# Performance work log

Hardware: AMD Instinct MI355X
Metric: run time of the kernel (lower is better)

Reference implementation:

```python
import jax, jax.numpy as jnp
import numpy as np

B, S, D = 8, 1024, 768
H = 12
DH = D // H  # 64


def setup_inputs() -> dict:
    key = jax.random.key(0)
    ks = jax.random.split(key, 9)
    s = 0.02
    return {
        "x": jax.random.normal(ks[0], (B, S, D), dtype=jnp.float32),
        # per-head QKV projections stacked over heads: [H, D, DH]
        "Wq": jax.random.normal(ks[1], (H, D, DH), dtype=jnp.float32) * s,
        "bq": jax.random.normal(ks[2], (H, DH), dtype=jnp.float32) * s,
        "Wk": jax.random.normal(ks[3], (H, D, DH), dtype=jnp.float32) * s,
        "bk": jax.random.normal(ks[4], (H, DH), dtype=jnp.float32) * s,
        "Wv": jax.random.normal(ks[5], (H, D, DH), dtype=jnp.float32) * s,
        "bv": jax.random.normal(ks[6], (H, DH), dtype=jnp.float32) * s,
        # output projection: [D, D] (applied as x @ Wo + bo)
        "Wo": jax.random.normal(ks[7], (D, D), dtype=jnp.float32) * s,
        "bo": jax.random.normal(ks[8], (D,), dtype=jnp.float32) * s,
    }


def reference(x, Wq, bq, Wk, bk, Wv, bv, Wo, bo):
    # Per-head linear projections, vectorized over heads -> [B, H, S, DH]
    q = jnp.einsum("bsd,hde->bhse", x, Wq) + bq[None, :, None, :]
    k = jnp.einsum("bsd,hde->bhse", x, Wk) + bk[None, :, None, :]
    v = jnp.einsum("bsd,hde->bhse", x, Wv) + bv[None, :, None, :]
    scale = 1.0 / jnp.sqrt(jnp.asarray(DH, dtype=q.dtype))
    scores = jnp.einsum("bhse,bhte->bhst", q, k) * scale  # [B,H,S,S]
    probs = jax.nn.softmax(scores, axis=-1)  # dropout p=0 (eval)
    out = jnp.einsum("bhst,bhte->bhse", probs, v)  # [B,H,S,DH]
    # concat heads (head order matches ModuleList order) -> [B,S,D]
    out = out.transpose(0, 2, 1, 3).reshape(B, S, D)
    return out @ Wo + bo
```

## Files before the change

### kernel.cpp

```cpp
#include <hip/hip_runtime.h>
#include <math.h>

#define BB 8
#define SS 1024
#define DD 768
#define HH 12
#define DHH 64
#define BSS (BB*SS)
#define NQKV 2304

typedef _Float16 half8 __attribute__((ext_vector_type(8)));
typedef _Float16 half4 __attribute__((ext_vector_type(4)));
typedef float    f32x4 __attribute__((ext_vector_type(4)));

__device__ __forceinline__ void glds16(const _Float16* g, _Float16* l)
{
    __builtin_amdgcn_global_load_lds(
        (const __attribute__((address_space(1))) uint32_t*)(g),
        (__attribute__((address_space(3))) uint32_t*)(l),
        16, 0, 0);
}

__global__ __launch_bounds__(256)
void cast_x_f16(const float* __restrict__ x, _Float16* __restrict__ xh)
{
    int i = blockIdx.x * 256 + threadIdx.x;
    const float4* xp = (const float4*)x + (size_t)i * 2;
    float4 u = xp[0], v = xp[1];
    half8 h = { (_Float16)u.x, (_Float16)u.y, (_Float16)u.z, (_Float16)u.w,
                (_Float16)v.x, (_Float16)v.y, (_Float16)v.z, (_Float16)v.w };
    ((half8*)xh)[i] = h;
}

__device__ __forceinline__
void transpose_tile(const float* __restrict__ src, _Float16* __restrict__ dst,
                    int d0, int n_outer, int base_mul, int row_stride, int tid)
{
    __shared__ float T[64][65];
    const size_t base = (size_t)n_outer * base_mul;
    {
        int dl = tid >> 2, c0 = (tid & 3) * 16;
        const float* p = src + base + (size_t)(d0 + dl) * row_stride + c0;
#pragma unroll
        for (int m = 0; m < 4; ++m) {
            float4 f = *(const float4*)(p + m * 4);
            T[dl][c0 + m*4 + 0] = f.x;
            T[dl][c0 + m*4 + 1] = f.y;
            T[dl][c0 + m*4 + 2] = f.z;
            T[dl][c0 + m*4 + 3] = f.w;
        }
    }
    __syncthreads();
    {
        int e = tid >> 2, c = tid & 3;
        half8 lo, hi;
#pragma unroll
        for (int i = 0; i < 8; ++i) {
            lo[i] = (_Float16)T[c*16 + i][e];
            hi[i] = (_Float16)T[c*16 + 8 + i][e];
        }
        _Float16* q = dst + ((size_t)n_outer * 64 + e) * DD + d0 + c * 16;
        *(half8*)q = lo;
        *(half8*)(q + 8) = hi;
    }
}

__global__ __launch_bounds__(256)
void transpose_all(const float* __restrict__ Wq, const float* __restrict__ Wk,
                   const float* __restrict__ Wv, const float* __restrict__ Wo,
                   _Float16* __restrict__ Wt, _Float16* __restrict__ Wot)
{
    const int z = blockIdx.z;
    const float* src;
    _Float16* dst;
    int base_mul, row_stride;
    if (z < 3) {
        src = (z == 0) ? Wq : (z == 1) ? Wk : Wv;
        dst = Wt + (size_t)z * DD * DD;
        base_mul = DD * DHH; row_stride = DHH;
    } else {
        src = Wo; dst = Wot;
        base_mul = 64; row_stride = DD;
    }
    transpose_tile(src, dst, blockIdx.x * 64, blockIdx.y, base_mul, row_stride,
                   threadIdx.x);
}

__global__ __launch_bounds__(256)
void gemm_qkv_stacked(const _Float16* __restrict__ Xh, const _Float16* __restrict__ Wt,
                      const float* __restrict__ bq, const float* __restrict__ bk,
                      const float* __restrict__ bv,
                      _Float16* __restrict__ qo, _Float16* __restrict__ ko,
                      _Float16* __restrict__ vto)
{
    __shared__ _Float16 Ash[128][32];
    __shared__ _Float16 Bsh[128][32];

    const int b = blockIdx.x;
    const int c  = b & 7;
    const int g  = b >> 3;
    const int n_t = g % 18;
    const int m_t = (g / 18) * 8 + c;
    const int m0 = m_t * 128;
    const int n0 = n_t * 128;

    const int tid  = threadIdx.x;
    const int wave = tid >> 6;
    const int lane = tid & 63;
    const int l16  = tid & 15;
    const int quad = (tid >> 4) & 3;
    const int wy = wave >> 1;
    const int wx = wave & 1;

    const _Float16* ap = Xh + (size_t)(m0 + 32 * wave + (lane >> 2)) * DD + (lane & 3) * 8;
    const _Float16* bp = Wt + (size_t)(n0 + 32 * wave + (lane >> 2)) * DD + (lane & 3) * 8;
    _Float16* ldsA0 = &Ash[32 * wave][0];
    _Float16* ldsA1 = &Ash[32 * wave + 16][0];
    _Float16* ldsB0 = &Bsh[32 * wave][0];
    _Float16* ldsB1 = &Bsh[32 * wave + 16][0];

    f32x4 acc[4][4];
#pragma unroll
    for (int i = 0; i < 4; ++i)
#pragma unroll
        for (int j = 0; j < 4; ++j) acc[i][j] = (f32x4){0.f, 0.f, 0.f, 0.f};

    for (int k0 = 0; k0 < DD; k0 += 32) {
        __syncthreads();
        glds16(ap, ldsA0);
        glds16(ap + 16 * DD, ldsA1);
        glds16(bp, ldsB0);
        glds16(bp + 16 * DD, ldsB1);
        ap += 32; bp += 32;
        __syncthreads();

        half8 a[4], bf[4];
#pragma unroll
        for (int i = 0; i < 4; ++i)
            a[i] = *(const half8*)&Ash[wy * 64 + i * 16 + l16][quad * 8];
#pragma unroll
        for (int j = 0; j < 4; ++j)
            bf[j] = *(const half8*)&Bsh[wx * 64 + j * 16 + l16][quad * 8];
#pragma unroll
        for (int i = 0; i < 4; ++i)
#pragma unroll
            for (int j = 0; j < 4; ++j)
                acc[i][j] = __builtin_amdgcn_mfma_f32_16x16x32_f16(a[i], bf[j], acc[i][j], 0, 0, 0);
    }

    const int w = n0 / 768;
    const float* bp_ = (w == 0) ? bq : (w == 1) ? bk : bv;
    const int nb = n0 - w * 768 + wx * 64;
    const float qscale = (w == 0) ? 0.125f : 1.0f;

#pragma unroll
    for (int i = 0; i < 4; ++i) {
#pragma unroll
        for (int r = 0; r < 4; ++r) {
            int row = m0 + wy * 64 + i * 16 + quad * 4 + r;
            int b_ = row >> 10;
            int s  = row & (SS - 1);
#pragma unroll
            for (int j = 0; j < 4; ++j) {
                int nl = nb + j * 16 + l16;
                int h = nl >> 6, e = nl & 63;
                float val = (acc[i][j][r] + bp_[nl]) * qscale;
                if (w == 0)
                    qo[((size_t)(b_ * HH + h) * SS + s) * DHH + e] = (_Float16)val;
                else if (w == 1)
                    ko[((size_t)(b_ * HH + h) * SS + s) * DHH + e] = (_Float16)val;
                else
                    vto[((size_t)(b_ * HH + h) * DHH + e) * SS + s] = (_Float16)val;
            }
        }
    }
}

__global__ __launch_bounds__(256)
void gemm_out_f16(const _Float16* __restrict__ Ah, const _Float16* __restrict__ Bt,
                  const float* __restrict__ bias, float* __restrict__ out)
{
    __shared__ _Float16 Ash[128][32];
    __shared__ _Float16 Bsh[128][32];

    const int m0 = blockIdx.x * 128;
    const int n0 = blockIdx.y * 128;
    const int tid  = threadIdx.x;
    const int wave = tid >> 6;
    const int lane = tid & 63;
    const int l16  = tid & 15;
    const int quad = (tid >> 4) & 3;
    const int wy = wave >> 1;
    const int wx = wave & 1;

    const _Float16* ap = Ah + (size_t)(m0 + 32 * wave + (lane >> 2)) * DD + (lane & 3) * 8;
    const _Float16* bp = Bt + (size_t)(n0 + 32 * wave + (lane >> 2)) * DD + (lane & 3) * 8;
    _Float16* ldsA0 = &Ash[32 * wave][0];
    _Float16* ldsA1 = &Ash[32 * wave + 16][0];
    _Float16* ldsB0 = &Bsh[32 * wave][0];
    _Float16* ldsB1 = &Bsh[32 * wave + 16][0];

    f32x4 acc[4][4];
#pragma unroll
    for (int i = 0; i < 4; ++i)
#pragma unroll
        for (int j = 0; j < 4; ++j) acc[i][j] = (f32x4){0.f, 0.f, 0.f, 0.f};

    for (int k0 = 0; k0 < DD; k0 += 32) {
        __syncthreads();
        glds16(ap, ldsA0);
        glds16(ap + 16 * DD, ldsA1);
        glds16(bp, ldsB0);
        glds16(bp + 16 * DD, ldsB1);
        ap += 32; bp += 32;
        __syncthreads();

        half8 a[4], bf[4];
#pragma unroll
        for (int i = 0; i < 4; ++i)
            a[i] = *(const half8*)&Ash[wy * 64 + i * 16 + l16][quad * 8];
#pragma unroll
        for (int j = 0; j < 4; ++j)
            bf[j] = *(const half8*)&Bsh[wx * 64 + j * 16 + l16][quad * 8];
#pragma unroll
        for (int i = 0; i < 4; ++i)
#pragma unroll
            for (int j = 0; j < 4; ++j)
                acc[i][j] = __builtin_amdgcn_mfma_f32_16x16x32_f16(a[i], bf[j], acc[i][j], 0, 0, 0);
    }

#pragma unroll
    for (int i = 0; i < 4; ++i) {
#pragma unroll
        for (int r = 0; r < 4; ++r) {
            int row = m0 + wy * 64 + i * 16 + quad * 4 + r;
#pragma unroll
            for (int j = 0; j < 4; ++j) {
                int col = n0 + wx * 64 + j * 16 + l16;
                out[(size_t)row * DD + col] = acc[i][j][r] + bias[col];
            }
        }
    }
}

__global__ __launch_bounds__(256)
void attn_f16(const _Float16* __restrict__ qh, const _Float16* __restrict__ kh,
              const _Float16* __restrict__ vt, _Float16* __restrict__ ctxh)
{
    const int bh  = blockIdx.x;
    const int q0  = blockIdx.y * 64;
    const int tid = threadIdx.x;
    const int wave = tid >> 6;
    const int lane = tid & 63;
    const int l16  = tid & 15;
    const int quad = (tid >> 4) & 3;

    __shared__ _Float16 Qs[64][64];
    __shared__ _Float16 Ks[64][64];
    __shared__ _Float16 Vt[64][64];
    __shared__ _Float16 Pt[4][16][72];

    const _Float16* qb  = qh + ((size_t)bh * SS + q0) * DHH;
    const _Float16* kb  = kh + (size_t)bh * SS * DHH;
    const _Float16* vtb = vt + (size_t)bh * DHH * SS;

    const int srow = 16 * wave + (lane >> 3);
    const int scol = (lane & 7) * 8;
    const _Float16* qp = qb + (size_t)srow * DHH + scol;
    const _Float16* kp = kb + (size_t)srow * DHH + scol;
    const _Float16* vp = vtb + (size_t)srow * SS + scol;

    glds16(qp, &Qs[16 * wave][0]);
    glds16(qp + 8 * DHH, &Qs[16 * wave + 8][0]);
    __syncthreads();

    const half8 qlo = *(const half8*)&Qs[wave * 16 + l16][quad * 8];
    const half8 qhi = *(const half8*)&Qs[wave * 16 + l16][32 + quad * 8];

    f32x4 o[4];
    float lacc = 0.f;
#pragma unroll
    for (int j = 0; j < 4; ++j) o[j] = (f32x4){0.f, 0.f, 0.f, 0.f};

    for (int kt = 0; kt < SS; kt += 64) {
        __syncthreads();
        glds16(kp, &Ks[16 * wave][0]);
        glds16(kp + 8 * DHH, &Ks[16 * wave + 8][0]);
        glds16(vp, &Vt[16 * wave][0]);
        glds16(vp + 8 * SS, &Vt[16 * wave + 8][0]);
        kp += 64 * DHH;
        vp += 64;
        __syncthreads();

#pragma unroll
        for (int f = 0; f < 4; ++f) {
            half8 klo = *(const half8*)&Ks[f * 16 + l16][quad * 8];
            half8 khi = *(const half8*)&Ks[f * 16 + l16][32 + quad * 8];
            f32x4 z = (f32x4){0.f, 0.f, 0.f, 0.f};
            z = __builtin_amdgcn_mfma_f32_16x16x32_f16(klo, qlo, z, 0, 0, 0);
            z = __builtin_amdgcn_mfma_f32_16x16x32_f16(khi, qhi, z, 0, 0, 0);
            half4 pk;
#pragma unroll
            for (int r = 0; r < 4; ++r) {
                float p = __expf(z[r]);
                lacc += p;
                pk[r] = (_Float16)p;
            }
            *(half4*)&Pt[wave][l16][f * 16 + quad * 4] = pk;
        }

        half8 pl = *(const half8*)&Pt[wave][l16][quad * 8];
        half8 ph = *(const half8*)&Pt[wave][l16][32 + quad * 8];

#pragma unroll
        for (int j = 0; j < 4; ++j) {
            half8 vlo = *(const half8*)&Vt[j * 16 + l16][quad * 8];
            half8 vhi = *(const half8*)&Vt[j * 16 + l16][32 + quad * 8];
            o[j] = __builtin_amdgcn_mfma_f32_16x16x32_f16(pl, vlo, o[j], 0, 0, 0);
            o[j] = __builtin_amdgcn_mfma_f32_16x16x32_f16(ph, vhi, o[j], 0, 0, 0);
        }
    }

    float lr = lacc;
    lr += __shfl_xor(lr, 16);
    lr += __shfl_xor(lr, 32);

    const int b_ = bh / HH;
    const int h_ = bh % HH;
#pragma unroll
    for (int r = 0; r < 4; ++r) {
        float invl = 1.f / __shfl(lr, quad * 4 + r, 16);
        int s_ = q0 + wave * 16 + quad * 4 + r;
        _Float16* orow = ctxh + ((size_t)(b_ * SS + s_)) * DD + h_ * DHH;
#pragma unroll
        for (int j = 0; j < 4; ++j)
            orow[j * 16 + l16] = (_Float16)(o[j][r] * invl);
    }
}

extern "C" void kernel_launch(void* const* d_in, const int* in_sizes, int n_in,
                              void* d_out, int out_size, void* d_ws, size_t ws_size,
                              hipStream_t stream)
{
    const float* x  = (const float*)d_in[0];
    const float* Wq = (const float*)d_in[1];
    const float* bq = (const float*)d_in[2];
    const float* Wk = (const float*)d_in[3];
    const float* bk = (const float*)d_in[4];
    const float* Wv = (const float*)d_in[5];
    const float* bv = (const float*)d_in[6];
    const float* Wo = (const float*)d_in[7];
    const float* bo = (const float*)d_in[8];
    float* out = (float*)d_out;

    const size_t xe = (size_t)BSS * DD;
    const size_t we = (size_t)DD * DD;
    _Float16* Xh   = (_Float16*)d_ws;
    _Float16* Wt   = Xh  + xe;
    _Float16* Wot  = Wt  + (size_t)3 * we;
    _Float16* qhb  = Wot + we;
    _Float16* khb  = qhb + xe;
    _Float16* vtb  = khb + xe;
    _Float16* ctxh = vtb + xe;

    cast_x_f16<<<xe / 8 / 256, 256, 0, stream>>>(x, Xh);

    dim3 tg(DD / 64, DD / 64, 4);
    transpose_all<<<tg, 256, 0, stream>>>(Wq, Wk, Wv, Wo, Wt, Wot);

    gemm_qkv_stacked<<<(BSS / 128) * (NQKV / 128), 256, 0, stream>>>(
        Xh, Wt, bq, bk, bv, qhb, khb, vtb);

    dim3 ag(BB * HH, SS / 64);
    attn_f16<<<ag, 256, 0, stream>>>(qhb, khb, vtb, ctxh);

    dim3 gg(BSS / 128, DD / 128);
    gemm_out_f16<<<gg, 256, 0, stream>>>(ctxh, Wot, bo, out);
}
```

Before: 240.1 us.

## Load GEMM and attention operands directly from global memory into registers

Drops the LDS staging and the per-iteration block barriers in both GEMMs and in the attention kernel. Each wave now reads its MFMA fragments straight from global memory, with register double-buffering to prefetch the next K slice. The output GEMM tile shrinks to 64 rows and launch bounds request 3 blocks per CU for occupancy. The cost is lost data sharing across waves: each A/B and K/V element is fetched from global or L2 several times, and the 16-byte per-lane row-strided loads may coalesce poorly.

```diff
diff --git a/kernel.cpp b/kernel.cpp
--- a/kernel.cpp
+++ b/kernel.cpp
@@ -12,14 +12,6 @@
 typedef _Float16 half8 __attribute__((ext_vector_type(8)));
 typedef _Float16 half4 __attribute__((ext_vector_type(4)));
 typedef float    f32x4 __attribute__((ext_vector_type(4)));
-
-__device__ __forceinline__ void glds16(const _Float16* g, _Float16* l)
-{
-    __builtin_amdgcn_global_load_lds(
-        (const __attribute__((address_space(1))) uint32_t*)(g),
-        (__attribute__((address_space(3))) uint32_t*)(l),
-        16, 0, 0);
-}
 
 __global__ __launch_bounds__(256)
 void cast_x_f16(const float* __restrict__ x, _Float16* __restrict__ xh)
@@ -86,16 +78,13 @@
                    threadIdx.x);
 }
 
-__global__ __launch_bounds__(256)
-void gemm_qkv_stacked(const _Float16* __restrict__ Xh, const _Float16* __restrict__ Wt,
-                      const float* __restrict__ bq, const float* __restrict__ bk,
-                      const float* __restrict__ bv,
-                      _Float16* __restrict__ qo, _Float16* __restrict__ ko,
-                      _Float16* __restrict__ vto)
-{
-    __shared__ _Float16 Ash[128][32];
-    __shared__ _Float16 Bsh[128][32];
-
+__global__ __launch_bounds__(256, 3)
+void gemm_qkv_direct(const _Float16* __restrict__ Xh, const _Float16* __restrict__ Wt,
+                     const float* __restrict__ bq, const float* __restrict__ bk,
+                     const float* __restrict__ bv,
+                     _Float16* __restrict__ qo, _Float16* __restrict__ ko,
+                     _Float16* __restrict__ vto)
+{
     const int b = blockIdx.x;
     const int c  = b & 7;
     const int g  = b >> 3;
@@ -106,18 +95,13 @@
 
     const int tid  = threadIdx.x;
     const int wave = tid >> 6;
-    const int lane = tid & 63;
     const int l16  = tid & 15;
     const int quad = (tid >> 4) & 3;
     const int wy = wave >> 1;
     const int wx = wave & 1;
 
-    const _Float16* ap = Xh + (size_t)(m0 + 32 * wave + (lane >> 2)) * DD + (lane & 3) * 8;
-    const _Float16* bp = Wt + (size_t)(n0 + 32 * wave + (lane >> 2)) * DD + (lane & 3) * 8;
-    _Float16* ldsA0 = &Ash[32 * wave][0];
-    _Float16* ldsA1 = &Ash[32 * wave + 16][0];
-    _Float16* ldsB0 = &Bsh[32 * wave][0];
-    _Float16* ldsB1 = &Bsh[32 * wave + 16][0];
+    const _Float16* abase = Xh + (size_t)(m0 + wy * 64 + l16) * DD + quad * 8;
+    const _Float16* bbase = Wt + (size_t)(n0 + wx * 64 + l16) * DD + quad * 8;
 
     f32x4 acc[4][4];
 #pragma unroll
@@ -125,27 +109,31 @@
 #pragma unroll
         for (int j = 0; j < 4; ++j) acc[i][j] = (f32x4){0.f, 0.f, 0.f, 0.f};
 
-    for (int k0 = 0; k0 < DD; k0 += 32) {
-        __syncthreads();
-        glds16(ap, ldsA0);
-        glds16(ap + 16 * DD, ldsA1);
-        glds16(bp, ldsB0);
-        glds16(bp + 16 * DD, ldsB1);
-        ap += 32; bp += 32;
-        __syncthreads();
-
-        half8 a[4], bf[4];
-#pragma unroll
-        for (int i = 0; i < 4; ++i)
-            a[i] = *(const half8*)&Ash[wy * 64 + i * 16 + l16][quad * 8];
-#pragma unroll
-        for (int j = 0; j < 4; ++j)
-            bf[j] = *(const half8*)&Bsh[wx * 64 + j * 16 + l16][quad * 8];
+    half8 a[4], bf[4];
+#pragma unroll
+    for (int i = 0; i < 4; ++i) {
+        a[i]  = *(const half8*)(abase + (size_t)i * 16 * DD);
+        bf[i] = *(const half8*)(bbase + (size_t)i * 16 * DD);
+    }
+
+    for (int k0 = 32; k0 <= DD; k0 += 32) {
+        half8 an[4], bn[4];
+        if (k0 < DD) {
+#pragma unroll
+            for (int i = 0; i < 4; ++i) {
+                an[i] = *(const half8*)(abase + (size_t)i * 16 * DD + k0);
+                bn[i] = *(const half8*)(bbase + (size_t)i * 16 * DD + k0);
+            }
+        }
 #pragma unroll
         for (int i = 0; i < 4; ++i)
 #pragma unroll
             for (int j = 0; j < 4; ++j)
                 acc[i][j] = __builtin_amdgcn_mfma_f32_16x16x32_f16(a[i], bf[j], acc[i][j], 0, 0, 0);
+        if (k0 < DD) {
+#pragma unroll
+            for (int i = 0; i < 4; ++i) { a[i] = an[i]; bf[i] = bn[i]; }
+        }
     }
 
     const int w = n0 / 768;
@@ -176,64 +164,60 @@
     }
 }
 
-__global__ __launch_bounds__(256)
-void gemm_out_f16(const _Float16* __restrict__ Ah, const _Float16* __restrict__ Bt,
-                  const float* __restrict__ bias, float* __restrict__ out)
-{
-    __shared__ _Float16 Ash[128][32];
-    __shared__ _Float16 Bsh[128][32];
-
-    const int m0 = blockIdx.x * 128;
+__global__ __launch_bounds__(256, 3)
+void gemm_out_direct(const _Float16* __restrict__ Ah, const _Float16* __restrict__ Bt,
+                     const float* __restrict__ bias, float* __restrict__ out)
+{
+    const int m0 = blockIdx.x * 64;
     const int n0 = blockIdx.y * 128;
     const int tid  = threadIdx.x;
     const int wave = tid >> 6;
-    const int lane = tid & 63;
     const int l16  = tid & 15;
     const int quad = (tid >> 4) & 3;
     const int wy = wave >> 1;
     const int wx = wave & 1;
 
-    const _Float16* ap = Ah + (size_t)(m0 + 32 * wave + (lane >> 2)) * DD + (lane & 3) * 8;
-    const _Float16* bp = Bt + (size_t)(n0 + 32 * wave + (lane >> 2)) * DD + (lane & 3) * 8;
-    _Float16* ldsA0 = &Ash[32 * wave][0];
-    _Float16* ldsA1 = &Ash[32 * wave + 16][0];
-    _Float16* ldsB0 = &Bsh[32 * wave][0];
-    _Float16* ldsB1 = &Bsh[32 * wave + 16][0];
-
-    f32x4 acc[4][4];
-#pragma unroll
-    for (int i = 0; i < 4; ++i)
+    const _Float16* abase = Ah + (size_t)(m0 + wy * 32 + l16) * DD + quad * 8;
+    const _Float16* bbase = Bt + (size_t)(n0 + wx * 64 + l16) * DD + quad * 8;
+
+    f32x4 acc[2][4];
+#pragma unroll
+    for (int i = 0; i < 2; ++i)
 #pragma unroll
         for (int j = 0; j < 4; ++j) acc[i][j] = (f32x4){0.f, 0.f, 0.f, 0.f};
 
-    for (int k0 = 0; k0 < DD; k0 += 32) {
-        __syncthreads();
-        glds16(ap, ldsA0);
-        glds16(ap + 16 * DD, ldsA1);
-        glds16(bp, ldsB0);
-        glds16(bp + 16 * DD, ldsB1);
-        ap += 32; bp += 32;
-        __syncthreads();
-
-        half8 a[4], bf[4];
-#pragma unroll
-        for (int i = 0; i < 4; ++i)
-            a[i] = *(const half8*)&Ash[wy * 64 + i * 16 + l16][quad * 8];
-#pragma unroll
-        for (int j = 0; j < 4; ++j)
-            bf[j] = *(const half8*)&Bsh[wx * 64 + j * 16 + l16][quad * 8];
-#pragma unroll
-        for (int i = 0; i < 4; ++i)
+    half8 a[2], bf[4];
+#pragma unroll
+    for (int i = 0; i < 2; ++i) a[i] = *(const half8*)(abase + (size_t)i * 16 * DD);
+#pragma unroll
+    for (int j = 0; j < 4; ++j) bf[j] = *(const half8*)(bbase + (size_t)j * 16 * DD);
+
+    for (int k0 = 32; k0 <= DD; k0 += 32) {
+        half8 an[2], bn[4];
+        if (k0 < DD) {
+#pragma unroll
+            for (int i = 0; i < 2; ++i) an[i] = *(const half8*)(abase + (size_t)i * 16 * DD + k0);
+#pragma unroll
+            for (int j = 0; j < 4; ++j) bn[j] = *(const half8*)(bbase + (size_t)j * 16 * DD + k0);
+        }
+#pragma unroll
+        for (int i = 0; i < 2; ++i)
 #pragma unroll
             for (int j = 0; j < 4; ++j)
                 acc[i][j] = __builtin_amdgcn_mfma_f32_16x16x32_f16(a[i], bf[j], acc[i][j], 0, 0, 0);
-    }
-
-#pragma unroll
-    for (int i = 0; i < 4; ++i) {
+        if (k0 < DD) {
+#pragma unroll
+            for (int i = 0; i < 2; ++i) a[i] = an[i];
+#pragma unroll
+            for (int j = 0; j < 4; ++j) bf[j] = bn[j];
+        }
+    }
+
+#pragma unroll
+    for (int i = 0; i < 2; ++i) {
 #pragma unroll
         for (int r = 0; r < 4; ++r) {
-            int row = m0 + wy * 64 + i * 16 + quad * 4 + r;
+            int row = m0 + wy * 32 + i * 16 + quad * 4 + r;
 #pragma unroll
             for (int j = 0; j < 4; ++j) {
                 int col = n0 + wx * 64 + j * 16 + l16;
@@ -251,31 +235,17 @@
     const int q0  = blockIdx.y * 64;
     const int tid = threadIdx.x;
     const int wave = tid >> 6;
-    const int lane = tid & 63;
     const int l16  = tid & 15;
     const int quad = (tid >> 4) & 3;
 
-    __shared__ _Float16 Qs[64][64];
-    __shared__ _Float16 Ks[64][64];
-    __shared__ _Float16 Vt[64][64];
     __shared__ _Float16 Pt[4][16][72];
 
-    const _Float16* qb  = qh + ((size_t)bh * SS + q0) * DHH;
-    const _Float16* kb  = kh + (size_t)bh * SS * DHH;
-    const _Float16* vtb = vt + (size_t)bh * DHH * SS;
-
-    const int srow = 16 * wave + (lane >> 3);
-    const int scol = (lane & 7) * 8;
-    const _Float16* qp = qb + (size_t)srow * DHH + scol;
-    const _Float16* kp = kb + (size_t)srow * DHH + scol;
-    const _Float16* vp = vtb + (size_t)srow * SS + scol;
-
-    glds16(qp, &Qs[16 * wave][0]);
-    glds16(qp + 8 * DHH, &Qs[16 * wave + 8][0]);
-    __syncthreads();
-
-    const half8 qlo = *(const half8*)&Qs[wave * 16 + l16][quad * 8];
-    const half8 qhi = *(const half8*)&Qs[wave * 16 + l16][32 + quad * 8];
+    const _Float16* qrow = qh + ((size_t)bh * SS + q0 + wave * 16 + l16) * DHH;
+    const half8 qlo = *(const half8*)(qrow + quad * 8);
+    const half8 qhi = *(const half8*)(qrow + 32 + quad * 8);
+
+    const _Float16* kptr = kh + ((size_t)bh * SS + l16) * DHH + quad * 8;
+    const _Float16* vptr = vt + ((size_t)bh * DHH + l16) * SS + quad * 8;
 
     f32x4 o[4];
     float lacc = 0.f;
@@ -283,22 +253,26 @@
     for (int j = 0; j < 4; ++j) o[j] = (f32x4){0.f, 0.f, 0.f, 0.f};
 
     for (int kt = 0; kt < SS; kt += 64) {
-        __syncthreads();
-        glds16(kp, &Ks[16 * wave][0]);
-        glds16(kp + 8 * DHH, &Ks[16 * wave + 8][0]);
-        glds16(vp, &Vt[16 * wave][0]);
-        glds16(vp + 8 * SS, &Vt[16 * wave + 8][0]);
-        kp += 64 * DHH;
-        vp += 64;
-        __syncthreads();
-
+        half8 kl[4], khv[4];
 #pragma unroll
         for (int f = 0; f < 4; ++f) {
-            half8 klo = *(const half8*)&Ks[f * 16 + l16][quad * 8];
-            half8 khi = *(const half8*)&Ks[f * 16 + l16][32 + quad * 8];
+            const _Float16* kp = kptr + (size_t)(kt + f * 16) * DHH;
+            kl[f]  = *(const half8*)kp;
+            khv[f] = *(const half8*)(kp + 32);
+        }
+        half8 vl[4], vh[4];
+#pragma unroll
+        for (int j = 0; j < 4; ++j) {
+            const _Float16* vp = vptr + (size_t)j * 16 * SS + kt;
+            vl[j] = *(const half8*)vp;
+            vh[j] = *(const half8*)(vp + 32);
+        }
+
+#pragma unroll
+        for (int f = 0; f < 4; ++f) {
             f32x4 z = (f32x4){0.f, 0.f, 0.f, 0.f};
-            z = __builtin_amdgcn_mfma_f32_16x16x32_f16(klo, qlo, z, 0, 0, 0);
-            z = __builtin_amdgcn_mfma_f32_16x16x32_f16(khi, qhi, z, 0, 0, 0);
+            z = __builtin_amdgcn_mfma_f32_16x16x32_f16(kl[f], qlo, z, 0, 0, 0);
+            z = __builtin_amdgcn_mfma_f32_16x16x32_f16(khv[f], qhi, z, 0, 0, 0);
             half4 pk;
 #pragma unroll
             for (int r = 0; r < 4; ++r) {
@@ -314,10 +288,8 @@
 
 #pragma unroll
         for (int j = 0; j < 4; ++j) {
-            half8 vlo = *(const half8*)&Vt[j * 16 + l16][quad * 8];
-            half8 vhi = *(const half8*)&Vt[j * 16 + l16][32 + quad * 8];
-            o[j] = __builtin_amdgcn_mfma_f32_16x16x32_f16(pl, vlo, o[j], 0, 0, 0);
-            o[j] = __builtin_amdgcn_mfma_f32_16x16x32_f16(ph, vhi, o[j], 0, 0, 0);
+            o[j] = __builtin_amdgcn_mfma_f32_16x16x32_f16(pl, vl[j], o[j], 0, 0, 0);
+            o[j] = __builtin_amdgcn_mfma_f32_16x16x32_f16(ph, vh[j], o[j], 0, 0, 0);
         }
     }
 
@@ -368,12 +340,12 @@
     dim3 tg(DD / 64, DD / 64, 4);
     transpose_all<<<tg, 256, 0, stream>>>(Wq, Wk, Wv, Wo, Wt, Wot);
 
-    gemm_qkv_stacked<<<(BSS / 128) * (NQKV / 128), 256, 0, stream>>>(
+    gemm_qkv_direct<<<(BSS / 128) * (NQKV / 128), 256, 0, stream>>>(
         Xh, Wt, bq, bk, bv, qhb, khb, vtb);
 
     dim3 ag(BB * HH, SS / 64);
     attn_f16<<<ag, 256, 0, stream>>>(qhb, khb, vtb, ctxh);
 
-    dim3 gg(BSS / 128, DD / 128);
-    gemm_out_f16<<<gg, 256, 0, stream>>>(ctxh, Wot, bo, out);
-}
+    dim3 gg(BSS / 64, DD / 128);
+    gemm_out_direct<<<gg, 256, 0, stream>>>(ctxh, Wot, bo, out);
+}
```

Result: slower. 467.7 us (+94.8%).

## Double-buffer LDS tiles in GEMMs and attention, widen attention blocks

Applied to the files above, without the earlier changes.

The QKV GEMM, output GEMM and attention kernels now use two LDS buffers. Each loop iteration prefetches the next K tile with async global-to-LDS loads while MFMAs run on the current tile, so each iteration needs one barrier instead of two. The attention kernel grows to 512 threads and 128 queries per block, which lets more query rows share each staged K/V tile; Q fragments are now read straight from global memory. The output GEMM tile shrinks to 128x64 to launch more blocks. In exchange, LDS use per block roughly doubles, which can lower occupancy.

```diff
diff --git a/kernel.cpp b/kernel.cpp
--- a/kernel.cpp
+++ b/kernel.cpp
@@ -93,8 +93,8 @@
                       _Float16* __restrict__ qo, _Float16* __restrict__ ko,
                       _Float16* __restrict__ vto)
 {
-    __shared__ _Float16 Ash[128][32];
-    __shared__ _Float16 Bsh[128][32];
+    __shared__ _Float16 Ash[2][128][32];
+    __shared__ _Float16 Bsh[2][128][32];
 
     const int b = blockIdx.x;
     const int c  = b & 7;
@@ -114,10 +114,6 @@
 
     const _Float16* ap = Xh + (size_t)(m0 + 32 * wave + (lane >> 2)) * DD + (lane & 3) * 8;
     const _Float16* bp = Wt + (size_t)(n0 + 32 * wave + (lane >> 2)) * DD + (lane & 3) * 8;
-    _Float16* ldsA0 = &Ash[32 * wave][0];
-    _Float16* ldsA1 = &Ash[32 * wave + 16][0];
-    _Float16* ldsB0 = &Bsh[32 * wave][0];
-    _Float16* ldsB1 = &Bsh[32 * wave + 16][0];
 
     f32x4 acc[4][4];
 #pragma unroll
@@ -125,27 +121,34 @@
 #pragma unroll
         for (int j = 0; j < 4; ++j) acc[i][j] = (f32x4){0.f, 0.f, 0.f, 0.f};
 
+    glds16(ap, &Ash[0][32 * wave][0]);
+    glds16(ap + 16 * DD, &Ash[0][32 * wave + 16][0]);
+    glds16(bp, &Bsh[0][32 * wave][0]);
+    glds16(bp + 16 * DD, &Bsh[0][32 * wave + 16][0]);
+
+    int cur = 0;
     for (int k0 = 0; k0 < DD; k0 += 32) {
         __syncthreads();
-        glds16(ap, ldsA0);
-        glds16(ap + 16 * DD, ldsA1);
-        glds16(bp, ldsB0);
-        glds16(bp + 16 * DD, ldsB1);
-        ap += 32; bp += 32;
-        __syncthreads();
+        if (k0 + 32 < DD) {
+            glds16(ap + k0 + 32, &Ash[cur ^ 1][32 * wave][0]);
+            glds16(ap + k0 + 32 + 16 * DD, &Ash[cur ^ 1][32 * wave + 16][0]);
+            glds16(bp + k0 + 32, &Bsh[cur ^ 1][32 * wave][0]);
+            glds16(bp + k0 + 32 + 16 * DD, &Bsh[cur ^ 1][32 * wave + 16][0]);
+        }
 
         half8 a[4], bf[4];
 #pragma unroll
         for (int i = 0; i < 4; ++i)
-            a[i] = *(const half8*)&Ash[wy * 64 + i * 16 + l16][quad * 8];
+            a[i] = *(const half8*)&Ash[cur][wy * 64 + i * 16 + l16][quad * 8];
 #pragma unroll
         for (int j = 0; j < 4; ++j)
-            bf[j] = *(const half8*)&Bsh[wx * 64 + j * 16 + l16][quad * 8];
+            bf[j] = *(const half8*)&Bsh[cur][wx * 64 + j * 16 + l16][quad * 8];
 #pragma unroll
         for (int i = 0; i < 4; ++i)
 #pragma unroll
             for (int j = 0; j < 4; ++j)
                 acc[i][j] = __builtin_amdgcn_mfma_f32_16x16x32_f16(a[i], bf[j], acc[i][j], 0, 0, 0);
+        cur ^= 1;
     }
 
     const int w = n0 / 768;
@@ -180,11 +183,11 @@
 void gemm_out_f16(const _Float16* __restrict__ Ah, const _Float16* __restrict__ Bt,
                   const float* __restrict__ bias, float* __restrict__ out)
 {
-    __shared__ _Float16 Ash[128][32];
-    __shared__ _Float16 Bsh[128][32];
+    __shared__ _Float16 Ash[2][128][32];
+    __shared__ _Float16 Bsh[2][64][32];
 
     const int m0 = blockIdx.x * 128;
-    const int n0 = blockIdx.y * 128;
+    const int n0 = blockIdx.y * 64;
     const int tid  = threadIdx.x;
     const int wave = tid >> 6;
     const int lane = tid & 63;
@@ -194,39 +197,40 @@
     const int wx = wave & 1;
 
     const _Float16* ap = Ah + (size_t)(m0 + 32 * wave + (lane >> 2)) * DD + (lane & 3) * 8;
-    const _Float16* bp = Bt + (size_t)(n0 + 32 * wave + (lane >> 2)) * DD + (lane & 3) * 8;
-    _Float16* ldsA0 = &Ash[32 * wave][0];
-    _Float16* ldsA1 = &Ash[32 * wave + 16][0];
-    _Float16* ldsB0 = &Bsh[32 * wave][0];
-    _Float16* ldsB1 = &Bsh[32 * wave + 16][0];
-
-    f32x4 acc[4][4];
+    const _Float16* bp = Bt + (size_t)(n0 + 16 * wave + (lane >> 2)) * DD + (lane & 3) * 8;
+
+    f32x4 acc[4][2];
 #pragma unroll
     for (int i = 0; i < 4; ++i)
 #pragma unroll
-        for (int j = 0; j < 4; ++j) acc[i][j] = (f32x4){0.f, 0.f, 0.f, 0.f};
-
+        for (int j = 0; j < 2; ++j) acc[i][j] = (f32x4){0.f, 0.f, 0.f, 0.f};
+
+    glds16(ap, &Ash[0][32 * wave][0]);
+    glds16(ap + 16 * DD, &Ash[0][32 * wave + 16][0]);
+    glds16(bp, &Bsh[0][16 * wave][0]);
+
+    int cur = 0;
     for (int k0 = 0; k0 < DD; k0 += 32) {
         __syncthreads();
-        glds16(ap, ldsA0);
-        glds16(ap + 16 * DD, ldsA1);
-        glds16(bp, ldsB0);
-        glds16(bp + 16 * DD, ldsB1);
-        ap += 32; bp += 32;
-        __syncthreads();
-
-        half8 a[4], bf[4];
+        if (k0 + 32 < DD) {
+            glds16(ap + k0 + 32, &Ash[cur ^ 1][32 * wave][0]);
+            glds16(ap + k0 + 32 + 16 * DD, &Ash[cur ^ 1][32 * wave + 16][0]);
+            glds16(bp + k0 + 32, &Bsh[cur ^ 1][16 * wave][0]);
+        }
+
+        half8 a[4], bf[2];
 #pragma unroll
         for (int i = 0; i < 4; ++i)
-            a[i] = *(const half8*)&Ash[wy * 64 + i * 16 + l16][quad * 8];
-#pragma unroll
-        for (int j = 0; j < 4; ++j)
-            bf[j] = *(const half8*)&Bsh[wx * 64 + j * 16 + l16][quad * 8];
+            a[i] = *(const half8*)&Ash[cur][wy * 64 + i * 16 + l16][quad * 8];
+#pragma unroll
+        for (int j = 0; j < 2; ++j)
+            bf[j] = *(const half8*)&Bsh[cur][wx * 32 + j * 16 + l16][quad * 8];
 #pragma unroll
         for (int i = 0; i < 4; ++i)
 #pragma unroll
-            for (int j = 0; j < 4; ++j)
+            for (int j = 0; j < 2; ++j)
                 acc[i][j] = __builtin_amdgcn_mfma_f32_16x16x32_f16(a[i], bf[j], acc[i][j], 0, 0, 0);
+        cur ^= 1;
     }
 
 #pragma unroll
@@ -235,67 +239,57 @@
         for (int r = 0; r < 4; ++r) {
             int row = m0 + wy * 64 + i * 16 + quad * 4 + r;
 #pragma unroll
-            for (int j = 0; j < 4; ++j) {
-                int col = n0 + wx * 64 + j * 16 + l16;
+            for (int j = 0; j < 2; ++j) {
+                int col = n0 + wx * 32 + j * 16 + l16;
                 out[(size_t)row * DD + col] = acc[i][j][r] + bias[col];
             }
         }
     }
 }
 
-__global__ __launch_bounds__(256)
+__global__ __launch_bounds__(512)
 void attn_f16(const _Float16* __restrict__ qh, const _Float16* __restrict__ kh,
               const _Float16* __restrict__ vt, _Float16* __restrict__ ctxh)
 {
     const int bh  = blockIdx.x;
-    const int q0  = blockIdx.y * 64;
+    const int q0  = blockIdx.y * 128;
     const int tid = threadIdx.x;
     const int wave = tid >> 6;
     const int lane = tid & 63;
     const int l16  = tid & 15;
     const int quad = (tid >> 4) & 3;
 
-    __shared__ _Float16 Qs[64][64];
-    __shared__ _Float16 Ks[64][64];
-    __shared__ _Float16 Vt[64][64];
-    __shared__ _Float16 Pt[4][16][72];
-
-    const _Float16* qb  = qh + ((size_t)bh * SS + q0) * DHH;
-    const _Float16* kb  = kh + (size_t)bh * SS * DHH;
-    const _Float16* vtb = vt + (size_t)bh * DHH * SS;
-
-    const int srow = 16 * wave + (lane >> 3);
-    const int scol = (lane & 7) * 8;
-    const _Float16* qp = qb + (size_t)srow * DHH + scol;
-    const _Float16* kp = kb + (size_t)srow * DHH + scol;
-    const _Float16* vp = vtb + (size_t)srow * SS + scol;
-
-    glds16(qp, &Qs[16 * wave][0]);
-    glds16(qp + 8 * DHH, &Qs[16 * wave + 8][0]);
-    __syncthreads();
-
-    const half8 qlo = *(const half8*)&Qs[wave * 16 + l16][quad * 8];
-    const half8 qhi = *(const half8*)&Qs[wave * 16 + l16][32 + quad * 8];
+    __shared__ _Float16 Ks[2][64][64];
+    __shared__ _Float16 Vt[2][64][64];
+    __shared__ _Float16 Pt[8][16][72];
+
+    const _Float16* qrow = qh + ((size_t)bh * SS + q0 + wave * 16 + l16) * DHH;
+    const half8 qlo = *(const half8*)(qrow + quad * 8);
+    const half8 qhi = *(const half8*)(qrow + 32 + quad * 8);
+
+    const _Float16* kp = kh + ((size_t)bh * SS + 8 * wave + (lane >> 3)) * DHH + (lane & 7) * 8;
+    const _Float16* vp = vt + ((size_t)bh * DHH + 8 * wave + (lane >> 3)) * SS + (lane & 7) * 8;
 
     f32x4 o[4];
     float lacc = 0.f;
 #pragma unroll
     for (int j = 0; j < 4; ++j) o[j] = (f32x4){0.f, 0.f, 0.f, 0.f};
 
+    glds16(kp, &Ks[0][8 * wave][0]);
+    glds16(vp, &Vt[0][8 * wave][0]);
+
+    int cur = 0;
     for (int kt = 0; kt < SS; kt += 64) {
         __syncthreads();
-        glds16(kp, &Ks[16 * wave][0]);
-        glds16(kp + 8 * DHH, &Ks[16 * wave + 8][0]);
-        glds16(vp, &Vt[16 * wave][0]);
-        glds16(vp + 8 * SS, &Vt[16 * wave + 8][0]);
-        kp += 64 * DHH;
-        vp += 64;
-        __syncthreads();
+        if (kt + 64 < SS) {
+            glds16(kp + (size_t)(kt + 64) * DHH, &Ks[cur ^ 1][8 * wave][0]);
+            glds16(vp + kt + 64, &Vt[cur ^ 1][8 * wave][0]);
+        }
 
 #pragma unroll
         for (int f = 0; f < 4; ++f) {
-            half8 klo = *(const half8*)&Ks[f * 16 + l16][quad * 8];
-            half8 khi = *(const half8*)&Ks[f * 16 + l16][32 + quad * 8];
+            half8 klo = *(const half8*)&Ks[cur][f * 16 + l16][quad * 8];
+            half8 khi = *(const half8*)&Ks[cur][f * 16 + l16][32 + quad * 8];
             f32x4 z = (f32x4){0.f, 0.f, 0.f, 0.f};
             z = __builtin_amdgcn_mfma_f32_16x16x32_f16(klo, qlo, z, 0, 0, 0);
             z = __builtin_amdgcn_mfma_f32_16x16x32_f16(khi, qhi, z, 0, 0, 0);
@@ -314,11 +308,12 @@
 
 #pragma unroll
         for (int j = 0; j < 4; ++j) {
-            half8 vlo = *(const half8*)&Vt[j * 16 + l16][quad * 8];
-            half8 vhi = *(const half8*)&Vt[j * 16 + l16][32 + quad * 8];
+            half8 vlo = *(const half8*)&Vt[cur][j * 16 + l16][quad * 8];
+            half8 vhi = *(const half8*)&Vt[cur][j * 16 + l16][32 + quad * 8];
             o[j] = __builtin_amdgcn_mfma_f32_16x16x32_f16(pl, vlo, o[j], 0, 0, 0);
             o[j] = __builtin_amdgcn_mfma_f32_16x16x32_f16(ph, vhi, o[j], 0, 0, 0);
         }
+        cur ^= 1;
     }
 
     float lr = lacc;
@@ -371,9 +366,9 @@
     gemm_qkv_stacked<<<(BSS / 128) * (NQKV / 128), 256, 0, stream>>>(
         Xh, Wt, bq, bk, bv, qhb, khb, vtb);
 
-    dim3 ag(BB * HH, SS / 64);
-    attn_f16<<<ag, 256, 0, stream>>>(qhb, khb, vtb, ctxh);
-
-    dim3 gg(BSS / 128, DD / 128);
+    dim3 ag(BB * HH, SS / 128);
+    attn_f16<<<ag, 512, 0, stream>>>(qhb, khb, vtb, ctxh);
+
+    dim3 gg(BSS / 128, DD / 64);
     gemm_out_f16<<<gg, 256, 0, stream>>>(ctxh, Wot, bo, out);
 }
```

Result: no change. 237.0 us (-1.3%).
